# Optimization experiments

Measured on AMD Instinct MI355X. Metric: run time of the kernel, lower is better.

The kernel has to match this reference:

```python
import jax, jax.numpy as jnp
import numpy as np

B, T, F = 64, 1024, 4
INF = jnp.float32(1e30)


def _dtw_cost(p, q):
    """Accumulated DTW cost matrix. p: [T1,2], q: [T2,2]. Returns C: [T1,T2].

    Recurrence C[i,j] = D[i,j] + min(C[i-1,j], C[i,j-1], C[i-1,j-1]).
    The within-row dependency c_j = d_j + min(a_j, c_{j-1}) (with
    a_j = min(C[i-1,j], C[i-1,j-1])) is a min-plus scan, solved in closed
    form: c_j = S_j + cummin_k<=j (a_k - S_{k-1}), S = cumsum(d).
    """
    # pairwise Euclidean distance (dtw.dtw2d uses 2D Euclidean)
    D = jnp.sqrt(jnp.sum((p[:, None, :] - q[None, :, :]) ** 2, axis=-1))  # [T1,T2]

    c0 = jnp.cumsum(D[0])  # first row: only left moves allowed

    def row(prev, d):
        shifted = jnp.concatenate([jnp.full((1,), INF, prev.dtype), prev[:-1]])
        a = jnp.minimum(prev, shifted)          # min(C[i-1,j], C[i-1,j-1])
        S = jnp.cumsum(d)
        Sprev = jnp.concatenate([jnp.zeros((1,), d.dtype), S[:-1]])
        m = jax.lax.associative_scan(jnp.minimum, a - Sprev)
        c = S + m
        return c, c

    _, rest = jax.lax.scan(row, c0, D[1:])
    return jnp.concatenate([c0[None, :], rest], axis=0)


def _dtw_path(C):
    """Backtrace alignment path from C. Returns (a, b, valid) each [T1+T2-1]."""
    T1, T2 = C.shape
    L = T1 + T2 - 1

    def step(carry, _):
        i, j, done = carry
        at0 = (i == 0) & (j == 0)
        cd = jnp.where((i > 0) & (j > 0), C[i - 1, j - 1], INF)
        cu = jnp.where(i > 0, C[i - 1, j], INF)
        cl = jnp.where(j > 0, C[i, j - 1], INF)
        k = jnp.argmin(jnp.stack([cd, cu, cl]))  # diag preferred on ties
        di = jnp.where(k == 2, 0, 1)
        dj = jnp.where(k == 1, 0, 1)
        ni = jnp.where(at0, 0, i - di)
        nj = jnp.where(at0, 0, j - dj)
        return (ni, nj, done | at0), (i, j, jnp.logical_not(done))

    init = (jnp.int32(T1 - 1), jnp.int32(T2 - 1), jnp.bool_(False))
    _, (a, b, valid) = jax.lax.scan(step, init, None, length=L)
    return a, b, valid


def _single_loss(pred, targ, subcoef):
    # DTW alignment computed on (x, y) basis, detached (torch runs it in numpy)
    p = jax.lax.stop_gradient(pred[:, :2])
    q = jax.lax.stop_gradient(targ[:, :2])
    C = _dtw_cost(p, q)
    a, b, valid = _dtw_path(C)
    # gather aligned points on loss_indices = [0, 1], L1 loss weighted by subcoef
    pg = pred[a, :2]  # [L, 2]
    tg = targ[b, :2]
    w = valid[:, None].astype(pred.dtype)
    return jnp.sum(jnp.abs(pg - tg) * subcoef[None, :] * w)


def setup_inputs() -> dict:
    key = jax.random.key(0)
    k1, k2 = jax.random.split(key)
    preds = jax.random.normal(k1, (B, T, F), dtype=jnp.float32)
    targs = jax.random.normal(k2, (B, T, F), dtype=jnp.float32)
    subcoef = jnp.ones((2,), dtype=jnp.float32)
    return {"preds": preds, "targs": targs, "subcoef": subcoef}


def reference(preds, targs, subcoef):
    losses = jax.vmap(lambda p, t: _single_loss(p, t, subcoef))(preds, targs)
    return jnp.sum(losses)
```

## Files before the change

kernel.cpp:

```cpp
#include <hip/hip_runtime.h>

#define TT   1024
#define NW   34
#define NPH  (NW + 21)
#define FINF 1e30f

template<bool A> struct BoolC { static constexpr bool value = A; };


__device__ __forceinline__ float dpp_shr1_old(float oldv, float x) {
    return __int_as_float(__builtin_amdgcn_update_dpp(
        __float_as_int(oldv), __float_as_int(x), 0x138, 0xF, 0xF, false));
}

__global__ __launch_bounds__(512) void dtw_forward(
    const float* __restrict__ preds,
    const float* __restrict__ targs,
    uint2* __restrict__ dirs)
{
    __shared__ float2 qsh[TT];
    __shared__ float  mbox[7][TT];

    const int tid  = threadIdx.x;
    const int w    = tid >> 6;
    const int lane = tid & 63;
    const int b    = blockIdx.x;

    for (int k = tid; k < TT; k += 512) {
        float4 t4 = ((const float4*)targs)[(size_t)b * TT + k];
        qsh[k] = make_float2(t4.x, t4.y);
    }
    for (int k = tid; k < 7 * TT; k += 512) ((float*)mbox)[k] = FINF;

    float px0, py0, px1, py1;
    {
        const int row0 = w * 128 + 2 * lane;
        float4 pv = ((const float4*)preds)[(size_t)b * TT + row0];
        px0 = pv.x; py0 = pv.y;
        float4 pw = ((const float4*)preds)[(size_t)b * TT + row0 + 1];
        px1 = pw.x; py1 = pw.y;
    }
    __syncthreads();

    const float* src = (w > 0) ? mbox[w - 1] : nullptr;
    float*       dst = (w < 7) ? mbox[w]     : nullptr;

    float cur0 = FINF, cur1 = FINF, uprev = FINF, ucur = FINF;
    unsigned au0 = 0, ad0 = 0, au1 = 0, ad1 = 0;
    unsigned pau0 = 0, pad0 = 0, pau1 = 0, pad1 = 0;
    int pT = -1;

    const int bi  = 2 * w + (lane >> 5);
    const int rr0 = 2 * (lane & 31);
    const bool is63 = (lane == 63);

    for (int G = 0; G < NPH; ++G) {
        if (pT >= 0) {
            const size_t base = (size_t)((b * 16 + bi) * NW + pT) * 64 + rr0;
            *(uint4*)&dirs[base] =
                make_uint4(__builtin_bitreverse32(pau0), __builtin_bitreverse32(pad0),
                           __builtin_bitreverse32(pau1), __builtin_bitreverse32(pad1));
            pT = -1;
        }
        const int T = G - 3 * w;
        if ((unsigned)T < (unsigned)NW) {
            float bnd[33];
#pragma unroll
            for (int k = 0; k < 33; ++k) bnd[k] = FINF;
            if (w > 0) {
#pragma unroll
                for (int k = 0; k < 33; ++k) {
                    const int c = 32 * T + k;
                    if (c < TT) bnd[k] = src[c];
                }
            }
            if (T == 0) ucur = bnd[0];
            float qx[32], qy[32];
#pragma unroll
            for (int k = 0; k < 32; ++k) {
                float2 v = qsh[(32 * T + k - lane) & (TT - 1)];
                qx[k] = v.x; qy[k] = v.y;
            }
            float bq[32];
            auto body = [&](auto actc) {
                constexpr bool ACT = decltype(actc)::value;
#pragma unroll
                for (int k2 = 0; k2 < 32; ++k2) {
                    const int s = 32 * T + k2;
                    const float dx0 = px0 - qx[k2], dy0 = py0 - qy[k2];
                    const float d0 = __builtin_amdgcn_sqrtf(dx0 * dx0 + dy0 * dy0);
                    const float dx1 = px1 - qx[k2], dy1 = py1 - qy[k2];
                    const float d1 = __builtin_amdgcn_sqrtf(dx1 * dx1 + dy1 * dy1);

                    const float u = ucur;
                    float ba0 = fminf(fminf(u, cur0), uprev);
                    const unsigned bd0 = (uprev == ba0) ? 1u : 0u;
                    const unsigned bu0 = ((u <= cur0) ? 1u : 0u) | bd0;
                    if constexpr (ACT) ba0 = (ba0 > 9e29f) ? 0.0f : ba0;
                    const float v0 = d0 + ba0;
                    const float ba1 = fminf(fminf(v0, cur1), cur0);
                    const unsigned bd1 = (cur0 == ba1) ? 1u : 0u;
                    const unsigned bu1 = ((v0 <= cur1) ? 1u : 0u) | bd1;
                    const float v1 = d1 + ba1;

                    au0 = (au0 << 1) | bu0;  ad0 = (ad0 << 1) | bd0;
                    au1 = (au1 << 1) | bu1;  ad1 = (ad1 << 1) | bd1;

                    if constexpr (ACT) {
                        const bool act = (lane <= s);
                        cur0 = act ? v0 : cur0;
                        cur1 = act ? v1 : cur1;
                    } else {
                        cur0 = v0; cur1 = v1;
                    }
                    uprev = u;
                    bq[k2] = cur1;
                    ucur = dpp_shr1_old(bnd[k2 + 1], cur1);
                }
            };
            if (T < 2) body(BoolC<true>{}); else body(BoolC<false>{});

            if (is63 && w < 7) {
#pragma unroll
                for (int k2 = 0; k2 < 32; ++k2) {
                    const int c = 32 * T + k2 - 63;
                    if ((unsigned)c < 1024u) dst[c] = bq[k2];
                }
            }
            pau0 = au0; pad0 = ad0; pau1 = au1; pad1 = ad1; pT = T;
            au0 = ad0 = au1 = ad1 = 0u;
        }
        __syncthreads();
    }
    if (pT >= 0) {
        const size_t base = (size_t)((b * 16 + bi) * NW + pT) * 64 + rr0;
        *(uint4*)&dirs[base] =
            make_uint4(__builtin_bitreverse32(pau0), __builtin_bitreverse32(pad0),
                       __builtin_bitreverse32(pau1), __builtin_bitreverse32(pad1));
    }
}

__global__ __launch_bounds__(1024) void dtw_exits(
    const uint2* __restrict__ dirs,
    unsigned short* __restrict__ exitc)
{
    __shared__ uint2 raw[NW * 64];
    __shared__ unsigned nebit[64][32];
    __shared__ unsigned dgbit[64][32];

    const int tid = threadIdx.x;
    const int b = blockIdx.x >> 4, bi = blockIdx.x & 15;

    for (int i = tid; i < NW * 64; i += 1024)
        raw[i] = dirs[(size_t)(b * 16 + bi) * (NW * 64) + i];
    __syncthreads();
    for (int i = tid; i < 64 * 32; i += 1024) {
        const int rr = i >> 5, u = i & 31;
        const int o  = ((bi & 1) << 5) + (rr >> 1);
        const int T0 = u + (o >> 5), sh = o & 31;
        uint2 A  = raw[T0 * 64 + rr];
        uint2 Bv = raw[(T0 + 1) * 64 + rr];
        nebit[rr][u] = sh ? ((A.x >> sh) | (Bv.x << (32 - sh))) : A.x;
        dgbit[rr][u] = sh ? ((A.y >> sh) | (Bv.y << (32 - sh))) : A.y;
    }
    __syncthreads();

    int j = tid;
    for (int rr = 63; rr >= 0; --rr) {
        if (bi == 0 && rr == 0) { j = 0; break; }
        int u = j >> 5, m = j & 31;
        unsigned wv = nebit[rr][u] << (31 - m);
        while (wv == 0u && u > 0) { --u; wv = nebit[rr][u]; m = 31; }
        const int j2 = (wv == 0u) ? 0 : ((u << 5) + m - __builtin_clz(wv));
        const int diag = (int)((dgbit[rr][j2 >> 5] >> (j2 & 31)) & 1u);
        j = j2 - diag;
        if (j < 0) j = 0;
    }
    exitc[((size_t)(b * 16 + bi) << 10) + tid] = (unsigned short)j;
}

__global__ void dtw_entries(const unsigned short* __restrict__ exitc,
                            unsigned short* __restrict__ ent)
{
    const int b = threadIdx.x;
    int j = TT - 1;
    for (int bi = 15; bi >= 0; --bi) {
        ent[b * 16 + bi] = (unsigned short)j;
        j = exitc[((size_t)(b * 16 + bi) << 10) + j];
    }
}

__global__ __launch_bounds__(64) void dtw_loss(
    const float* __restrict__ preds,
    const float* __restrict__ targs,
    const float* __restrict__ subcoef,
    const uint2* __restrict__ dirs,
    const unsigned short* __restrict__ ent,
    float* __restrict__ out)
{
    __shared__ uint2 raw[NW * 64];
    __shared__ unsigned nebit[64][32];
    __shared__ unsigned dgbit[64][32];
    __shared__ float2 qsh[TT];
    __shared__ float2 psh[64];
    __shared__ unsigned recs[160];

    const int lane = threadIdx.x;
    const int b = blockIdx.x >> 4, bi = blockIdx.x & 15;

    for (int i = lane; i < NW * 64; i += 64)
        raw[i] = dirs[(size_t)(b * 16 + bi) * (NW * 64) + i];
    for (int k = lane; k < TT; k += 64) {
        float4 t4 = ((const float4*)targs)[(size_t)b * TT + k];
        qsh[k] = make_float2(t4.x, t4.y);
    }
    {
        float4 p4 = ((const float4*)preds)[(size_t)b * TT + bi * 64 + lane];
        psh[lane] = make_float2(p4.x, p4.y);
    }
    __syncthreads();
    for (int i = lane; i < 64 * 32; i += 64) {
        const int rr = i >> 5, u = i & 31;
        const int o  = ((bi & 1) << 5) + (rr >> 1);
        const int T0 = u + (o >> 5), sh = o & 31;
        uint2 A  = raw[T0 * 64 + rr];
        uint2 Bv = raw[(T0 + 1) * 64 + rr];
        nebit[rr][u] = sh ? ((A.x >> sh) | (Bv.x << (32 - sh))) : A.x;
        dgbit[rr][u] = sh ? ((A.y >> sh) | (Bv.y << (32 - sh))) : A.y;
    }
    __syncthreads();

    int j = ent[b * 16 + bi];
    int nrec = 0;
    for (int rr = 63; rr >= 0; --rr) {
        int j2;
        if (bi == 0 && rr == 0) j2 = 0;
        else {
            int u = j >> 5, m = j & 31;
            unsigned wv = nebit[rr][u] << (31 - m);
            while (wv == 0u && u > 0) { --u; wv = nebit[rr][u]; m = 31; }
            j2 = (wv == 0u) ? 0 : ((u << 5) + m - __builtin_clz(wv));
        }
        int c = j;
        for (;;) {
            int cl = (c - 31 > j2) ? (c - 31) : j2;
            if (lane == 0)
                recs[nrec] = ((unsigned)rr << 20) | ((unsigned)cl << 10) | (unsigned)c;
            ++nrec;
            if (cl == j2) break;
            c = cl - 1;
        }
        if (bi == 0 && rr == 0) j = 0;
        else {
            const int diag = (int)((dgbit[rr][j2 >> 5] >> (j2 & 31)) & 1u);
            j = j2 - diag;
            if (j < 0) j = 0;
        }
    }
    __syncthreads();

    const float sc0 = subcoef[0], sc1 = subcoef[1];
    float acc = 0.0f;
    for (int k = lane; k < nrec; k += 64) {
        unsigned rec = recs[k];
        int rr = (int)(rec >> 20), cl = (int)((rec >> 10) & 1023u), ch = (int)(rec & 1023u);
        float2 p = psh[rr];
        for (int c = cl; c <= ch; ++c) {
            float2 q = qsh[c];
            acc += fabsf(p.x - q.x) * sc0 + fabsf(p.y - q.y) * sc1;
        }
    }
    for (int o = 32; o; o >>= 1) acc += __shfl_down(acc, o);
    if (lane == 0) atomicAdd(out, acc);
}

extern "C" void kernel_launch(void* const* d_in, const int* in_sizes, int n_in,
                              void* d_out, int out_size, void* d_ws, size_t ws_size,
                              hipStream_t stream)
{
    const float* preds   = (const float*)d_in[0];
    const float* targs   = (const float*)d_in[1];
    const float* subcoef = (const float*)d_in[2];
    float* out = (float*)d_out;

    const int B = in_sizes[0] / (TT * 4);

    const size_t dirsBytes = (size_t)B * 16 * NW * 64 * sizeof(uint2);
    const size_t exitBytes = (size_t)B * 16 * 1024 * sizeof(unsigned short);
    uint2* dirs = (uint2*)d_ws;
    unsigned short* exitc = (unsigned short*)((char*)d_ws + dirsBytes);
    unsigned short* ent   = (unsigned short*)((char*)d_ws + dirsBytes + exitBytes);

    hipMemsetAsync(out, 0, sizeof(float), stream);
    dtw_forward<<<dim3(B), dim3(512), 0, stream>>>(preds, targs, dirs);
    dtw_exits<<<dim3(B * 16), dim3(1024), 0, stream>>>(dirs, exitc);
    dtw_entries<<<dim3(1), dim3(B), 0, stream>>>(exitc, ent);
    dtw_loss<<<dim3(B * 16), dim3(64), 0, stream>>>(preds, targs, subcoef, dirs, ent, out);
}
```

Baseline: 412.2 us.

## Process two column tiles per barrier phase and fold entry chaining into loss kernel

The forward wavefront kernel now handles 64 columns per phase instead of 32, with a skew of 2 phases per warp. This cuts the number of block-wide barriers from 55 to 31, at the cost of more registers for the boundary and q buffers. The separate single-block dtw_entries kernel is removed; each loss block walks the exit table itself to find its entry column, which drops one kernel launch but adds redundant serial loads per block.

New measurement: 424.6 us. 3.0% more time.

```diff
diff --git a/kernel.cpp b/kernel.cpp
--- a/kernel.cpp
+++ b/kernel.cpp
@@ -2,7 +2,8 @@
 
 #define TT   1024
 #define NW   34
-#define NPH  (NW + 21)
+#define NWP  17
+#define NPH  (NWP + 14)
 #define FINF 1e30f
 
 template<bool A> struct BoolC { static constexpr bool value = A; };
@@ -46,47 +47,65 @@
     float*       dst = (w < 7) ? mbox[w]     : nullptr;
 
     float cur0 = FINF, cur1 = FINF, uprev = FINF, ucur = FINF;
-    unsigned au0 = 0, ad0 = 0, au1 = 0, ad1 = 0;
-    unsigned pau0 = 0, pad0 = 0, pau1 = 0, pad1 = 0;
-    int pT = -1;
+    unsigned pA0 = 0, pA1 = 0, pA2 = 0, pA3 = 0;
+    unsigned pB0 = 0, pB1 = 0, pB2 = 0, pB3 = 0;
+    int pP = -1;
 
     const int bi  = 2 * w + (lane >> 5);
     const int rr0 = 2 * (lane & 31);
-    const bool is63 = (lane == 63);
+    const bool pub = (lane == 63) && (w < 7);
 
     for (int G = 0; G < NPH; ++G) {
-        if (pT >= 0) {
-            const size_t base = (size_t)((b * 16 + bi) * NW + pT) * 64 + rr0;
-            *(uint4*)&dirs[base] =
-                make_uint4(__builtin_bitreverse32(pau0), __builtin_bitreverse32(pad0),
-                           __builtin_bitreverse32(pau1), __builtin_bitreverse32(pad1));
-            pT = -1;
-        }
-        const int T = G - 3 * w;
-        if ((unsigned)T < (unsigned)NW) {
-            float bnd[33];
-#pragma unroll
-            for (int k = 0; k < 33; ++k) bnd[k] = FINF;
+        if (pP >= 0) {
+            const size_t base = (size_t)((b * 16 + bi) * NW + 2 * pP) * 64 + rr0;
+            *(uint4*)&dirs[base] = make_uint4(
+                __builtin_bitreverse32(pA0), __builtin_bitreverse32(pA1),
+                __builtin_bitreverse32(pA2), __builtin_bitreverse32(pA3));
+            *(uint4*)&dirs[base + 64] = make_uint4(
+                __builtin_bitreverse32(pB0), __builtin_bitreverse32(pB1),
+                __builtin_bitreverse32(pB2), __builtin_bitreverse32(pB3));
+            pP = -1;
+        }
+        const int P = G - 2 * w;
+        if ((unsigned)P < (unsigned)NWP) {
+            const int s0 = 64 * P;
+            float bndA[33], bndB[33];
+#pragma unroll
+            for (int k = 0; k < 33; ++k) { bndA[k] = FINF; bndB[k] = FINF; }
             if (w > 0) {
-#pragma unroll
-                for (int k = 0; k < 33; ++k) {
-                    const int c = 32 * T + k;
-                    if (c < TT) bnd[k] = src[c];
-                }
-            }
-            if (T == 0) ucur = bnd[0];
-            float qx[32], qy[32];
-#pragma unroll
-            for (int k = 0; k < 32; ++k) {
-                float2 v = qsh[(32 * T + k - lane) & (TT - 1)];
-                qx[k] = v.x; qy[k] = v.y;
-            }
+                if (P <= 14) {
+#pragma unroll
+                    for (int k = 0; k < 33; ++k) bndA[k] = src[s0 + k];
+#pragma unroll
+                    for (int k = 0; k < 33; ++k) bndB[k] = src[s0 + 32 + k];
+                } else {
+#pragma unroll
+                    for (int k = 0; k < 33; ++k) {
+                        if (s0 + k < TT)      bndA[k] = src[s0 + k];
+                        if (s0 + 32 + k < TT) bndB[k] = src[s0 + 32 + k];
+                    }
+                }
+            }
+            float qxA[32], qyA[32];
+            if (P >= 1 && P <= 15) {
+                const float2* qp = &qsh[s0 - lane];
+#pragma unroll
+                for (int k = 0; k < 32; ++k) { qxA[k] = qp[k].x; qyA[k] = qp[k].y; }
+            } else {
+#pragma unroll
+                for (int k = 0; k < 32; ++k) {
+                    float2 v = qsh[(s0 + k - lane) & (TT - 1)];
+                    qxA[k] = v.x; qyA[k] = v.y;
+                }
+            }
+            if (P == 0) ucur = bndA[0];
+            unsigned au0 = 0, ad0 = 0, au1 = 0, ad1 = 0;
             float bq[32];
-            auto body = [&](auto actc) {
+            auto half = [&](const float* bnd, const float* qx, const float* qy,
+                            int sbase, auto actc) {
                 constexpr bool ACT = decltype(actc)::value;
 #pragma unroll
                 for (int k2 = 0; k2 < 32; ++k2) {
-                    const int s = 32 * T + k2;
                     const float dx0 = px0 - qx[k2], dy0 = py0 - qy[k2];
                     const float d0 = __builtin_amdgcn_sqrtf(dx0 * dx0 + dy0 * dy0);
                     const float dx1 = px1 - qx[k2], dy1 = py1 - qy[k2];
@@ -103,11 +122,11 @@
                     const unsigned bu1 = ((v0 <= cur1) ? 1u : 0u) | bd1;
                     const float v1 = d1 + ba1;
 
-                    au0 = (au0 << 1) | bu0;  ad0 = (ad0 << 1) | bd0;
-                    au1 = (au1 << 1) | bu1;  ad1 = (ad1 << 1) | bd1;
+                    au0 = au0 + au0 + bu0;  ad0 = ad0 + ad0 + bd0;
+                    au1 = au1 + au1 + bu1;  ad1 = ad1 + ad1 + bd1;
 
                     if constexpr (ACT) {
-                        const bool act = (lane <= s);
+                        const bool act = (lane <= sbase + k2);
                         cur0 = act ? v0 : cur0;
                         cur1 = act ? v1 : cur1;
                     } else {
@@ -118,25 +137,51 @@
                     ucur = dpp_shr1_old(bnd[k2 + 1], cur1);
                 }
             };
-            if (T < 2) body(BoolC<true>{}); else body(BoolC<false>{});
-
-            if (is63 && w < 7) {
+            if (P == 0) half(bndA, qxA, qyA, 0, BoolC<true>{});
+            else        half(bndA, qxA, qyA, 0, BoolC<false>{});
+            pA0 = au0; pA1 = ad0; pA2 = au1; pA3 = ad1;
+            au0 = ad0 = au1 = ad1 = 0u;
+            if (pub) {
 #pragma unroll
                 for (int k2 = 0; k2 < 32; ++k2) {
-                    const int c = 32 * T + k2 - 63;
+                    const int c = s0 + k2 - 63;
                     if ((unsigned)c < 1024u) dst[c] = bq[k2];
                 }
             }
-            pau0 = au0; pad0 = ad0; pau1 = au1; pad1 = ad1; pT = T;
-            au0 = ad0 = au1 = ad1 = 0u;
+            float qxB[32], qyB[32];
+            if (P >= 1 && P <= 15) {
+                const float2* qp = &qsh[s0 + 32 - lane];
+#pragma unroll
+                for (int k = 0; k < 32; ++k) { qxB[k] = qp[k].x; qyB[k] = qp[k].y; }
+            } else {
+#pragma unroll
+                for (int k = 0; k < 32; ++k) {
+                    float2 v = qsh[(s0 + 32 + k - lane) & (TT - 1)];
+                    qxB[k] = v.x; qyB[k] = v.y;
+                }
+            }
+            if (P == 0) half(bndB, qxB, qyB, 32, BoolC<true>{});
+            else        half(bndB, qxB, qyB, 32, BoolC<false>{});
+            pB0 = au0; pB1 = ad0; pB2 = au1; pB3 = ad1;
+            if (pub) {
+#pragma unroll
+                for (int k2 = 0; k2 < 32; ++k2) {
+                    const int c = s0 + 32 + k2 - 63;
+                    if ((unsigned)c < 1024u) dst[c] = bq[k2];
+                }
+            }
+            pP = P;
         }
         __syncthreads();
     }
-    if (pT >= 0) {
-        const size_t base = (size_t)((b * 16 + bi) * NW + pT) * 64 + rr0;
-        *(uint4*)&dirs[base] =
-            make_uint4(__builtin_bitreverse32(pau0), __builtin_bitreverse32(pad0),
-                       __builtin_bitreverse32(pau1), __builtin_bitreverse32(pad1));
+    if (pP >= 0) {
+        const size_t base = (size_t)((b * 16 + bi) * NW + 2 * pP) * 64 + rr0;
+        *(uint4*)&dirs[base] = make_uint4(
+            __builtin_bitreverse32(pA0), __builtin_bitreverse32(pA1),
+            __builtin_bitreverse32(pA2), __builtin_bitreverse32(pA3));
+        *(uint4*)&dirs[base + 64] = make_uint4(
+            __builtin_bitreverse32(pB0), __builtin_bitreverse32(pB1),
+            __builtin_bitreverse32(pB2), __builtin_bitreverse32(pB3));
     }
 }
 
@@ -179,23 +224,12 @@
     exitc[((size_t)(b * 16 + bi) << 10) + tid] = (unsigned short)j;
 }
 
-__global__ void dtw_entries(const unsigned short* __restrict__ exitc,
-                            unsigned short* __restrict__ ent)
-{
-    const int b = threadIdx.x;
-    int j = TT - 1;
-    for (int bi = 15; bi >= 0; --bi) {
-        ent[b * 16 + bi] = (unsigned short)j;
-        j = exitc[((size_t)(b * 16 + bi) << 10) + j];
-    }
-}
-
 __global__ __launch_bounds__(64) void dtw_loss(
     const float* __restrict__ preds,
     const float* __restrict__ targs,
     const float* __restrict__ subcoef,
     const uint2* __restrict__ dirs,
-    const unsigned short* __restrict__ ent,
+    const unsigned short* __restrict__ exitc,
     float* __restrict__ out)
 {
     __shared__ uint2 raw[NW * 64];
@@ -228,9 +262,12 @@
         nebit[rr][u] = sh ? ((A.x >> sh) | (Bv.x << (32 - sh))) : A.x;
         dgbit[rr][u] = sh ? ((A.y >> sh) | (Bv.y << (32 - sh))) : A.y;
     }
-    __syncthreads();
-
-    int j = ent[b * 16 + bi];
+
+    int j = TT - 1;
+    for (int k = 15; k > bi; --k)
+        j = exitc[((size_t)(b * 16 + k) << 10) + j];
+    __syncthreads();
+
     int nrec = 0;
     for (int rr = 63; rr >= 0; --rr) {
         int j2;
@@ -286,14 +323,11 @@
     const int B = in_sizes[0] / (TT * 4);
 
     const size_t dirsBytes = (size_t)B * 16 * NW * 64 * sizeof(uint2);
-    const size_t exitBytes = (size_t)B * 16 * 1024 * sizeof(unsigned short);
     uint2* dirs = (uint2*)d_ws;
     unsigned short* exitc = (unsigned short*)((char*)d_ws + dirsBytes);
-    unsigned short* ent   = (unsigned short*)((char*)d_ws + dirsBytes + exitBytes);
 
     hipMemsetAsync(out, 0, sizeof(float), stream);
     dtw_forward<<<dim3(B), dim3(512), 0, stream>>>(preds, targs, dirs);
     dtw_exits<<<dim3(B * 16), dim3(1024), 0, stream>>>(dirs, exitc);
-    dtw_entries<<<dim3(1), dim3(B), 0, stream>>>(exitc, ent);
-    dtw_loss<<<dim3(B * 16), dim3(64), 0, stream>>>(preds, targs, subcoef, dirs, ent, out);
-}
+    dtw_loss<<<dim3(B * 16), dim3(64), 0, stream>>>(preds, targs, subcoef, dirs, exitc, out);
+}
```

## Replace all-start exit tracing with single-path per-batch traceback kernel

Applied to the files above, without the earlier changes.

The old exits kernel traced all 1024 starting columns through each of the 16 row bands, and a second kernel then chained the exits into per-band entry columns. The new single kernel per batch element traces only the actual path. One wavefront holds the band's bits in registers and reads them with readlane, while the other wavefronts realign the next band's direction bits into double-buffered shared memory. This removes redundant tracing work and one kernel launch, but makes the traceback serial per batch with only 64 blocks, so latency depends on a sequential chain. It also rewrites the bit-accumulation shifts as adds in the forward kernel.

Measured after the change: 449.2 us. +9.0%, slower.

```diff
diff --git a/kernel.cpp b/kernel.cpp
--- a/kernel.cpp
+++ b/kernel.cpp
@@ -11,6 +11,9 @@
 __device__ __forceinline__ float dpp_shr1_old(float oldv, float x) {
     return __int_as_float(__builtin_amdgcn_update_dpp(
         __float_as_int(oldv), __float_as_int(x), 0x138, 0xF, 0xF, false));
+}
+__device__ __forceinline__ unsigned rdlane(unsigned v, int l) {
+    return (unsigned)__builtin_amdgcn_readlane((int)v, l);
 }
 
 __global__ __launch_bounds__(512) void dtw_forward(
@@ -103,8 +106,8 @@
                     const unsigned bu1 = ((v0 <= cur1) ? 1u : 0u) | bd1;
                     const float v1 = d1 + ba1;
 
-                    au0 = (au0 << 1) | bu0;  ad0 = (ad0 << 1) | bd0;
-                    au1 = (au1 << 1) | bu1;  ad1 = (ad1 << 1) | bd1;
+                    au0 = au0 + au0 + bu0;  ad0 = ad0 + ad0 + bd0;
+                    au1 = au1 + au1 + bu1;  ad1 = ad1 + ad1 + bd1;
 
                     if constexpr (ACT) {
                         const bool act = (lane <= s);
@@ -140,54 +143,57 @@
     }
 }
 
-__global__ __launch_bounds__(1024) void dtw_exits(
+__global__ __launch_bounds__(512) void dtw_trace(
     const uint2* __restrict__ dirs,
-    unsigned short* __restrict__ exitc)
+    unsigned short* __restrict__ ent)
 {
-    __shared__ uint2 raw[NW * 64];
-    __shared__ unsigned nebit[64][32];
-    __shared__ unsigned dgbit[64][32];
-
-    const int tid = threadIdx.x;
-    const int b = blockIdx.x >> 4, bi = blockIdx.x & 15;
-
-    for (int i = tid; i < NW * 64; i += 1024)
-        raw[i] = dirs[(size_t)(b * 16 + bi) * (NW * 64) + i];
-    __syncthreads();
-    for (int i = tid; i < 64 * 32; i += 1024) {
-        const int rr = i >> 5, u = i & 31;
-        const int o  = ((bi & 1) << 5) + (rr >> 1);
-        const int T0 = u + (o >> 5), sh = o & 31;
-        uint2 A  = raw[T0 * 64 + rr];
-        uint2 Bv = raw[(T0 + 1) * 64 + rr];
-        nebit[rr][u] = sh ? ((A.x >> sh) | (Bv.x << (32 - sh))) : A.x;
-        dgbit[rr][u] = sh ? ((A.y >> sh) | (Bv.y << (32 - sh))) : A.y;
-    }
-    __syncthreads();
-
-    int j = tid;
-    for (int rr = 63; rr >= 0; --rr) {
-        if (bi == 0 && rr == 0) { j = 0; break; }
-        int u = j >> 5, m = j & 31;
-        unsigned wv = nebit[rr][u] << (31 - m);
-        while (wv == 0u && u > 0) { --u; wv = nebit[rr][u]; m = 31; }
-        const int j2 = (wv == 0u) ? 0 : ((u << 5) + m - __builtin_clz(wv));
-        const int diag = (int)((dgbit[rr][j2 >> 5] >> (j2 & 31)) & 1u);
-        j = j2 - diag;
-        if (j < 0) j = 0;
-    }
-    exitc[((size_t)(b * 16 + bi) << 10) + tid] = (unsigned short)j;
-}
-
-__global__ void dtw_entries(const unsigned short* __restrict__ exitc,
-                            unsigned short* __restrict__ ent)
-{
-    const int b = threadIdx.x;
+    __shared__ unsigned bits[2][64][64];
+
+    const int tid  = threadIdx.x;
+    const int w    = tid >> 6;
+    const int lane = tid & 63;
+    const int b    = blockIdx.x;
+
+    auto realign = [&](int band, int p, int tbase, int tstep) {
+        const size_t gbase = (size_t)(b * 16 + band) * (NW * 64);
+        for (int i = tbase; i < 2048; i += tstep) {
+            const int rr = i >> 5, u = i & 31;
+            const int o  = ((band & 1) << 5) + (rr >> 1);
+            const int T0 = u + (o >> 5), sh = o & 31;
+            uint2 A  = dirs[gbase + T0 * 64 + rr];
+            uint2 Bv = dirs[gbase + (T0 + 1) * 64 + rr];
+            bits[p][rr][u]      = sh ? ((A.x >> sh) | (Bv.x << (32 - sh))) : A.x;
+            bits[p][rr][32 + u] = sh ? ((A.y >> sh) | (Bv.y << (32 - sh))) : A.y;
+        }
+    };
+
+    realign(15, 1, tid, 512);
+    __syncthreads();
+
     int j = TT - 1;
-    for (int bi = 15; bi >= 0; --bi) {
-        ent[b * 16 + bi] = (unsigned short)j;
-        j = exitc[((size_t)(b * 16 + bi) << 10) + j];
-    }
+    for (int bi = 15; bi >= 1; --bi) {
+        const int p = bi & 1;
+        if (w == 0) {
+            if (lane == 0) ent[b * 16 + bi] = (unsigned short)j;
+            unsigned vv[64];
+#pragma unroll
+            for (int rr = 0; rr < 64; ++rr) vv[rr] = bits[p][rr][lane];
+#pragma unroll
+            for (int rr = 63; rr >= 0; --rr) {
+                int u = j >> 5, m = j & 31;
+                unsigned wv = rdlane(vv[rr], u) << (31 - m);
+                while (wv == 0u && u > 0) { --u; wv = rdlane(vv[rr], u); m = 31; }
+                const int j2 = (wv == 0u) ? 0 : ((u << 5) + m - __builtin_clz(wv));
+                const unsigned dgw = rdlane(vv[rr], 32 + (j2 >> 5));
+                j = j2 - (int)((dgw >> (j2 & 31)) & 1u);
+                if (j < 0) j = 0;
+            }
+        } else if (bi >= 2) {
+            realign(bi - 1, (bi - 1) & 1, tid - 64, 448);
+        }
+        __syncthreads();
+    }
+    if (tid == 0) ent[b * 16] = (unsigned short)j;
 }
 
 __global__ __launch_bounds__(64) void dtw_loss(
@@ -286,14 +292,11 @@
     const int B = in_sizes[0] / (TT * 4);
 
     const size_t dirsBytes = (size_t)B * 16 * NW * 64 * sizeof(uint2);
-    const size_t exitBytes = (size_t)B * 16 * 1024 * sizeof(unsigned short);
     uint2* dirs = (uint2*)d_ws;
-    unsigned short* exitc = (unsigned short*)((char*)d_ws + dirsBytes);
-    unsigned short* ent   = (unsigned short*)((char*)d_ws + dirsBytes + exitBytes);
+    unsigned short* ent = (unsigned short*)((char*)d_ws + dirsBytes);
 
     hipMemsetAsync(out, 0, sizeof(float), stream);
     dtw_forward<<<dim3(B), dim3(512), 0, stream>>>(preds, targs, dirs);
-    dtw_exits<<<dim3(B * 16), dim3(1024), 0, stream>>>(dirs, exitc);
-    dtw_entries<<<dim3(1), dim3(B), 0, stream>>>(exitc, ent);
+    dtw_trace<<<dim3(B), dim3(512), 0, stream>>>(dirs, ent);
     dtw_loss<<<dim3(B * 16), dim3(64), 0, stream>>>(preds, targs, subcoef, dirs, ent, out);
 }
```
